# Performance work log

Measured on AMD Instinct MI355X. Metric: run time of the kernel, lower is better.

The kernel has to match this reference:

```python
import jax, jax.numpy as jnp
import numpy as np
from jax import lax

N_CLASS = 21          # VOC: 20 foreground + background
SCORE_THRESH = 0.05   # 'evaluate' preset
NMS_THRESH = 0.3


def loc2bbox(src_bbox, loc):
    # src_bbox, loc: [N, 4] in (y1, x1, y2, x2) / (dy, dx, dh, dw)
    h = src_bbox[:, 2] - src_bbox[:, 0]
    w = src_bbox[:, 3] - src_bbox[:, 1]
    cy = src_bbox[:, 0] + 0.5 * h
    cx = src_bbox[:, 1] + 0.5 * w
    dy, dx, dh, dw = loc[:, 0], loc[:, 1], loc[:, 2], loc[:, 3]
    ncy = dy * h + cy
    ncx = dx * w + cx
    nh = jnp.exp(dh) * h
    nw = jnp.exp(dw) * w
    return jnp.stack([ncy - 0.5 * nh, ncx - 0.5 * nw,
                      ncy + 0.5 * nh, ncx + 0.5 * nw], axis=1)


def pairwise_iou(boxes):
    # boxes: [R, 4] (y1, x1, y2, x2) -> [R, R]
    area = (boxes[:, 2] - boxes[:, 0]) * (boxes[:, 3] - boxes[:, 1])
    ty1 = jnp.maximum(boxes[:, None, 0], boxes[None, :, 0])
    tx1 = jnp.maximum(boxes[:, None, 1], boxes[None, :, 1])
    ty2 = jnp.minimum(boxes[:, None, 2], boxes[None, :, 2])
    tx2 = jnp.minimum(boxes[:, None, 3], boxes[None, :, 3])
    inter = jnp.clip(ty2 - ty1, 0) * jnp.clip(tx2 - tx1, 0)
    union = area[:, None] + area[None, :] - inter
    return inter / jnp.maximum(union, 1e-10)


def nms_keep(boxes, scores):
    # boxes [R,4], scores [R] for one class. Returns bool keep mask [R]
    # (score-thresholded + greedy NMS), fixed shape (mask instead of gather).
    R = boxes.shape[0]
    valid = scores > SCORE_THRESH
    order = jnp.argsort(-scores)
    b = boxes[order]
    v = valid[order]
    suppress = pairwise_iou(b) > NMS_THRESH  # [R, R]
    idx = jnp.arange(R)

    def body(i, keep):
        sup_by_earlier = jnp.any(keep & suppress[:, i] & (idx < i))
        return keep.at[i].set(v[i] & ~sup_by_earlier)

    keep_sorted = lax.fori_loop(0, R, body, jnp.zeros((R,), bool))
    return jnp.zeros((R,), bool).at[order].set(keep_sorted)


def setup_inputs() -> dict:
    key = jax.random.key(0)
    k1, k2, k3, k4 = jax.random.split(key, 4)
    R = 2000
    size_h, size_w = 600, 800
    roi_cls_loc = jax.random.normal(k1, (R, N_CLASS * 4), jnp.float32)
    roi_scores = jax.random.normal(k2, (R, N_CLASS), jnp.float32)
    # valid (y1, x1, y2, x2) rois inside the image
    yx = jax.random.uniform(k3, (R, 2), jnp.float32) * jnp.array([size_h - 32.0, size_w - 32.0])
    hw = 16.0 + jax.random.uniform(k4, (R, 2), jnp.float32) * 128.0
    rois = jnp.concatenate([yx, yx + hw], axis=1)
    return {"roi_cls_loc": roi_cls_loc, "roi_scores": roi_scores,
            "rois": rois, "size_h": size_h, "size_w": size_w}


def reference(roi_cls_loc, roi_scores, rois, size_h, size_w):
    R = rois.shape[0]
    mean = jnp.tile(jnp.asarray([0.0, 0.0, 0.0, 0.0], roi_cls_loc.dtype), N_CLASS)
    std = jnp.tile(jnp.asarray([0.1, 0.1, 0.2, 0.2], roi_cls_loc.dtype), N_CLASS)
    loc = roi_cls_loc * std + mean                      # [R, 4*C]
    loc = loc.reshape(R * N_CLASS, 4)
    src = jnp.broadcast_to(rois[:, None, :], (R, N_CLASS, 4)).reshape(R * N_CLASS, 4)
    box = loc2bbox(src, loc).reshape(R, N_CLASS, 4)
    # clamp y coords (0,2) to [0, H], x coords (1,3) to [0, W]
    y = jnp.clip(box[..., 0::2], 0.0, float(size_h))
    x = jnp.clip(box[..., 1::2], 0.0, float(size_w))
    box = jnp.stack([y[..., 0], x[..., 0], y[..., 1], x[..., 1]], axis=-1)
    prob = jax.nn.softmax(roi_scores, axis=1)           # [R, C]
    # foreground classes only (skip background class 0)
    cls_box = jnp.transpose(box[:, 1:, :], (1, 0, 2))   # [C-1, R, 4]
    cls_prob = prob[:, 1:].T                            # [C-1, R]
    keep = jax.vmap(nms_keep)(lax.stop_gradient(cls_box),
                              lax.stop_gradient(cls_prob))  # [C-1, R] bool
    kept = keep.astype(box.dtype)[..., None]
    # fixed-shape detections: per-class boxes + score, zeroed where suppressed
    out = jnp.concatenate([cls_box * kept, cls_prob[..., None] * kept], axis=-1)
    return out  # [C-1, R, 5]
```

## Files before the change

### kernel.cpp

```cpp
#include <hip/hip_runtime.h>
#include <math.h>

#define NCLS 21
#define NCO 20
#define SUB 8
#define TPB 256
#define RCAP 2048
#define RMAX 2000
#define LDSW 7680
#define SCORE_THRESH 0.05f

typedef unsigned long long u64;
typedef unsigned int u32;
typedef unsigned short u16;

#define IOU_MID (20132661.0 / 67108864.0)

__device__ __forceinline__ u64 readlane64(u64 v, int l) {
    u32 lo = (u32)__builtin_amdgcn_readlane((int)(u32)v, l);
    u32 hi = (u32)__builtin_amdgcn_readlane((int)(u32)(v >> 32), l);
    return ((u64)hi << 32) | lo;
}
__device__ __forceinline__ float readlanef(float v, int l) {
    return __uint_as_float((u32)__builtin_amdgcn_readlane((int)__float_as_uint(v), l));
}
__device__ __forceinline__ u64 shflxor64(u64 v, int m) {
    u32 lo = (u32)__shfl_xor((int)(u32)v, m, 64);
    u32 hi = (u32)__shfl_xor((int)(u32)(v >> 32), m, 64);
    return ((u64)hi << 32) | lo;
}

__device__ __forceinline__ int coff(int ic, int nw) {
    return ((ic * nw - ((ic * (ic - 1)) >> 1)) << 6);
}

__device__ __forceinline__ void decode_box(
    const float* __restrict__ rois, const float* __restrict__ loc,
    int r, int cls, float sh, float sw,
    float& by1, float& bx1, float& by2, float& bx2)
{
    float4 rb = *(const float4*)(rois + r * 4);
    float y1 = rb.x, x1 = rb.y, y2 = rb.z, x2 = rb.w;
    float h = y2 - y1, w = x2 - x1;
    float cy = y1 + 0.5f * h, cx = x1 + 0.5f * w;
    float4 l4 = *(const float4*)(loc + r * (NCLS * 4) + cls * 4);
    float dy = l4.x * 0.1f, dx = l4.y * 0.1f;
    float dh = l4.z * 0.2f, dw = l4.w * 0.2f;
    float ncy = dy * h + cy, ncx = dx * w + cx;
    float nh = expf(dh) * h, nw = expf(dw) * w;
    by1 = fminf(fmaxf(ncy - 0.5f * nh, 0.f), sh);
    bx1 = fminf(fmaxf(ncx - 0.5f * nw, 0.f), sw);
    by2 = fminf(fmaxf(ncy + 0.5f * nh, 0.f), sh);
    bx2 = fminf(fmaxf(ncx + 0.5f * nw, 0.f), sw);
}

__device__ __forceinline__ float softmax_p(
    const float* __restrict__ scores, int r, int cls)
{
    const float* srow = scores + r * NCLS;
    float s[NCLS];
    float4 a0 = *(const float4*)(srow);
    float4 a1 = *(const float4*)(srow + 4);
    float4 a2 = *(const float4*)(srow + 8);
    float4 a3 = *(const float4*)(srow + 12);
    float4 a4 = *(const float4*)(srow + 16);
    s[0]=a0.x; s[1]=a0.y; s[2]=a0.z; s[3]=a0.w;
    s[4]=a1.x; s[5]=a1.y; s[6]=a1.z; s[7]=a1.w;
    s[8]=a2.x; s[9]=a2.y; s[10]=a2.z; s[11]=a2.w;
    s[12]=a3.x; s[13]=a3.y; s[14]=a3.z; s[15]=a3.w;
    s[16]=a4.x; s[17]=a4.y; s[18]=a4.z; s[19]=a4.w;
    s[20]=srow[20];
    float m = -INFINITY;
#pragma unroll
    for (int k = 0; k < NCLS; ++k) m = fmaxf(m, s[k]);
    float sum = 0.f, ec = 0.f;
#pragma unroll
    for (int k = 0; k < NCLS; ++k) {
        float e = expf(s[k] - m);
        sum += e;
        if (k == cls) ec = e;
    }
    return ec / sum;
}

__global__ __launch_bounds__(256) void keygen_kernel(
    const float* __restrict__ scores, u64* __restrict__ ukey,
    int* __restrict__ cntA, int R)
{
    __shared__ u64 lkey[256];
    __shared__ int cnt;
    const int t = threadIdx.x;
    const int c = blockIdx.x >> 3;
    const int s = blockIdx.x & 7;
    const int lane = t & 63;
    if (t == 0) cnt = 0;
    __syncthreads();
    const int rpb = (R + 7) >> 3;
    const int r0 = s * rpb, r1 = min(R, r0 + rpb);
    for (int r = r0 + t; r < r1; r += 256) {
        float p = softmax_p(scores, r, c + 1);
        bool valid = (p > SCORE_THRESH);
        u64 key = ((u64)(~__float_as_uint(p)) << 32) | (u32)r;
        u64 bal = __ballot(valid);
        if (bal) {
            int nb = (int)__popcll(bal);
            int base = 0;
            if (lane == 0) base = atomicAdd(&cnt, nb);
            base = __shfl(base, 0, 64);
            if (valid)
                lkey[base + (int)__popcll(bal & ((1ull << lane) - 1ull))] = key;
        }
    }
    __syncthreads();
    const int n = cnt;
    if (t == 0) cntA[(c << 3) | s] = n;
    for (int j = t; j < n; j += 256)
        ukey[((size_t)c << 11) + (s << 8) + j] = lkey[j];
}

__global__ __launch_bounds__(512) void rank_kernel(
    const float* __restrict__ loc, const float* __restrict__ rois,
    const int* __restrict__ ph, const int* __restrict__ pw,
    const u64* __restrict__ ukey, const int* __restrict__ cntA,
    u64* __restrict__ ord, int* __restrict__ nvv,
    float4* __restrict__ pbG, float* __restrict__ arG, int R)
{
    __shared__ __align__(16) u64 vkey[RCAP + 2];
    const int t = threadIdx.x;
    const int c = blockIdx.x >> 3;
    const int s = blockIdx.x & 7;
    const int wv = t >> 6, lane = t & 63;
    int nv = 0, bseg = 0, nseg = 0;
#pragma unroll
    for (int k = 0; k < 8; ++k) {
        int ck = cntA[(c << 3) | k];
        if (k < wv) bseg += ck;
        if (k == wv) nseg = ck;
        nv += ck;
    }
    for (int j = lane; j < nseg; j += 64)
        vkey[bseg + j] = ukey[((size_t)c << 11) + (wv << 8) + j];
    if (t == 0) vkey[nv] = ~0ull;
    __syncthreads();

    const int sl = (nv + 7) >> 3;
    const int i0 = s * sl;
    const int nmy = max(0, min(nv - i0, sl));
    if (t < nmy) {
        u64 kk = vkey[i0 + t];
        int rank = 0;
        const ulonglong2* vk2 = (const ulonglong2*)vkey;
        const int nj2 = (nv + 1) >> 1;
#pragma unroll 8
        for (int j = 0; j < nj2; ++j) {
            ulonglong2 kj = vk2[j];
            rank += (int)(kj.x < kk) + (int)(kj.y < kk);
        }
        const float sh = (float)(*ph), sw = (float)(*pw);
        int r = (int)(u32)kk;
        float b0, b1, b2, b3;
        decode_box(rois, loc, r, c + 1, sh, sw, b0, b1, b2, b3);
        ord[((size_t)c << 11) + rank] = kk;
        pbG[((size_t)c << 11) + rank] = make_float4(b0, b1, b2, b3);
        arG[((size_t)c << 11) + rank] = (b2 - b0) * (b3 - b1);
    }
    if (t == 0 && s == 0) nvv[c] = nv;
}

__global__ __launch_bounds__(512) void maskp_kernel(
    const float4* __restrict__ pbG, const float* __restrict__ arG,
    const int* __restrict__ nvv, u64* __restrict__ M)
{
    __shared__ float4 pb[RCAP];
    __shared__ float ar[RCAP];
    const int t = threadIdx.x;
    const int c = blockIdx.x >> 3;
    const int s = blockIdx.x & 7;
    const int lane = t & 63;
    const int nv = nvv[c];
    const int nw = (nv + 63) >> 6;
    for (int i = t; i < nv; i += 512) {
        pb[i] = pbG[((size_t)c << 11) + i];
        ar[i] = arG[((size_t)c << 11) + i];
    }
    __syncthreads();

    const int wid = (s << 3) | (t >> 6);
    const int ntasks = nw * (nw + 1) / 2;
    u64* Mc = M + ((size_t)c << 16);
    for (int task = wid; task < ntasks; task += SUB * 8) {
        int ic = 0, rm = task;
        while (rm >= nw - ic) { rm -= nw - ic; ++ic; }
        int v = ic + rm;
        int i = (ic << 6) + lane;
        float4 a = pb[i];
        float iarea = ar[i];
        float4 rj = pb[(v << 6) + lane];
        float ja_l = ar[(v << 6) + lane];
        int jcnt = min(64, nv - (v << 6));
        u64 m = 0;
        for (int jj = 0; jj < jcnt; ++jj) {
            float jy1 = readlanef(rj.x, jj);
            float jx1 = readlanef(rj.y, jj);
            float jy2 = readlanef(rj.z, jj);
            float jx2 = readlanef(rj.w, jj);
            float ja  = readlanef(ja_l, jj);
            float ty1 = fmaxf(a.x, jy1);
            float tx1 = fmaxf(a.y, jx1);
            float ty2 = fminf(a.z, jy2);
            float tx2 = fminf(a.w, jx2);
            float inter = fmaxf(ty2 - ty1, 0.f) * fmaxf(tx2 - tx1, 0.f);
            float uni = fmaxf(iarea + ja - inter, 1e-10f);
            if ((double)inter > IOU_MID * (double)uni) m |= 1ull << jj;
        }
        if (v == ic) m &= (lane < 63) ? (~0ull << (lane + 1)) : 0ull;
        int W = nw - ic;
        if (i < nv) Mc[coff(ic, nw) + lane * W + (v - ic)] = m;
    }
}

__global__ __launch_bounds__(TPB) void resolveout_kernel(
    const float* __restrict__ loc, const float* __restrict__ rois,
    const int* __restrict__ ph, const int* __restrict__ pw,
    const u64* __restrict__ ord, const int* __restrict__ nvv,
    const u64* __restrict__ M, float* __restrict__ out, int R)
{
    __shared__ u64 mlds[LDSW];
    __shared__ u64 keptw[32];
    const int t = threadIdx.x;
    const int c = blockIdx.x >> 3;
    const int s = blockIdx.x & 7;
    const int nv = nvv[c];
    const int nw = (nv + 63) >> 6;
    const u64* Mc = M + ((size_t)c << 16);
    const int S = coff(nw, nw);
    const bool lds_ok = (S <= LDSW);
    if (t < 32) keptw[t] = 0;

    if (lds_ok) {
        for (int base = 0; base < S; base += 2048) {
            u64 v[8];
#pragma unroll
            for (int j = 0; j < 8; ++j) {
                int k = base + (j << 8) + t;
                v[j] = (k < S) ? Mc[k] : 0ull;
            }
#pragma unroll
            for (int j = 0; j < 8; ++j) {
                int k = base + (j << 8) + t;
                if (k < S) mlds[k] = v[j];
            }
        }
    }
    __syncthreads();

    if (t < 64) {
        const int lane = t;
        auto core = [&](const auto* B) {
            u64 remreg = 0;
            for (int w = 0; w < nw; ++w) {
                const int W = nw - w;
                const int cb = coff(w, nw);
                int i = (w << 6) + lane;
                u64 cw = (i < nv) ? B[cb + lane * W] : 0ull;
                int remn = nv - (w << 6);
                u64 vb = (remn >= 64) ? ~0ull : ((1ull << remn) - 1ull);
                u64 cand = vb & ~readlane64(remreg, w);
                u64 X = cand;
                if (X) {
                    for (int it = 0; it < 64; ++it) {
                        u64 contrib = ((X >> lane) & 1ull) ? cw : 0ull;
#pragma unroll
                        for (int d = 1; d < 64; d <<= 1)
                            contrib |= shflxor64(contrib, d);
                        bool keep = ((cand >> lane) & 1ull) &&
                                    !((contrib >> lane) & 1ull);
                        u64 Xn = __ballot(keep);
                        if (Xn == X) break;
                        X = Xn;
                    }
                    if (lane == 0) keptw[w] = X;
                    bool lact = (lane > w) && (lane < nw);
                    u64 km = X, acc = 0;
                    while (km) {
                        int bs[8];
#pragma unroll
                        for (int g = 0; g < 8; ++g) {
                            bs[g] = km ? (__ffsll(km) - 1) : -1;
                            if (km) km &= km - 1;
                        }
                        u64 tmp[8];
#pragma unroll
                        for (int g = 0; g < 8; ++g)
                            tmp[g] = (bs[g] >= 0 && lact)
                                ? B[cb + bs[g] * W + (lane - w)] : 0ull;
#pragma unroll
                        for (int g = 0; g < 8; ++g) acc |= tmp[g];
                    }
                    if (lact) remreg |= acc;
                }
            }
        };
        if (lds_ok) core(mlds); else core(Mc);
    }
    __syncthreads();

    const int chunk = (R + 7) >> 3;
    const int r0 = s * chunk;
    const int r1 = min(R, r0 + chunk);
    float* slice = out + (size_t)c * R * 5;
    for (int k = r0 * 5 + t; k < r1 * 5; k += TPB) slice[k] = 0.f;
    __syncthreads();

    const float sh = (float)(*ph), sw = (float)(*pw);
    for (int i = t; i < nv; i += TPB) {
        if ((keptw[i >> 6] >> (i & 63)) & 1ull) {
            u64 key = ord[((size_t)c << 11) + i];
            int r = (int)(u32)key;
            if (r >= r0 && r < r1) {
                float v0, v1, v2, v3;
                decode_box(rois, loc, r, c + 1, sh, sw, v0, v1, v2, v3);
                float* p = slice + (size_t)r * 5;
                p[0] = v0; p[1] = v1; p[2] = v2; p[3] = v3;
                p[4] = __uint_as_float(~(u32)(key >> 32));
            }
        }
    }
}

#define NTH 1024
__global__ __launch_bounds__(NTH) void fused_kernel(
    const float* __restrict__ loc, const float* __restrict__ scores,
    const float* __restrict__ rois, const int* __restrict__ ph,
    const int* __restrict__ pw, float* __restrict__ out, int R)
{
    __shared__ u64 vkey[RMAX];
    __shared__ float2 p1[RMAX], p2[RMAX];
    __shared__ u64 chunk[64 * 33];
    __shared__ u64 rem[32];
    __shared__ int cnt;

    const int t = threadIdx.x;
    const int lane = t & 63;
    const int c = blockIdx.x + 1;
    const float sh = (float)(*ph), sw = (float)(*pw);

    if (t == 0) cnt = 0;
    if (t < 32) rem[t] = 0;
    __syncthreads();

    for (int r = t; r < R; r += NTH) {
        float p = softmax_p(scores, r, c);
        if (p > SCORE_THRESH) {
            int j = atomicAdd(&cnt, 1);
            vkey[j] = ((u64)(~__float_as_uint(p)) << 32) | (u32)r;
        }
    }
    __syncthreads();
    const int nv = cnt;
    const int nw = (nv + 63) >> 6;

    u64 kk0 = 0, kk1 = 0;
    int r0 = 0, r1 = 0;
    bool in0 = (t < nv), in1 = (t + NTH < nv);
    if (in0) kk0 = vkey[t];
    if (in1) kk1 = vkey[t + NTH];
#pragma unroll 8
    for (int i = 0; i < nv; ++i) {
        u64 k = vkey[i];
        r0 += (k < kk0);
        r1 += (k < kk1);
    }
    __syncthreads();

    for (int u = 0; u < 2; ++u) {
        bool act = u ? in1 : in0;
        if (act) {
            u64 kk = u ? kk1 : kk0;
            int rank = u ? r1 : r0;
            int r = (int)(kk & 0xffffffffu);
            float b0, b1, b2, b3;
            decode_box(rois, loc, r, c, sh, sw, b0, b1, b2, b3);
            vkey[rank] = kk;
            p1[rank] = make_float2(b0, b1);
            p2[rank] = make_float2(b2, b3);
        }
    }
    __syncthreads();

    for (int w = 0; w < nw; ++w) {
        int nwr = nw - w;
        u64 remw = rem[w];
        for (int task = t; task < (nwr << 6); task += NTH) {
            int vr = task >> 6, il = task & 63;
            int i = (w << 6) + il;
            u64 m = 0;
            if (i < nv && !((remw >> il) & 1ull)) {
                int v = w + vr;
                u64 rv = rem[v];
                if (~rv != 0ull) {
                    float2 a1 = p1[i], a2 = p2[i];
                    float iarea = (a2.x - a1.x) * (a2.y - a1.y);
                    int j0 = v << 6;
                    int jhi = min(64, nv - j0);
#pragma unroll 4
                    for (int jj = 0; jj < jhi; ++jj) {
                        float2 b1 = p1[j0 + jj], b2 = p2[j0 + jj];
                        float ty1 = fmaxf(a1.x, b1.x);
                        float tx1 = fmaxf(a1.y, b1.y);
                        float ty2 = fminf(a2.x, b2.x);
                        float tx2 = fminf(a2.y, b2.y);
                        float inter = fmaxf(ty2 - ty1, 0.f) * fmaxf(tx2 - tx1, 0.f);
                        float jarea = (b2.x - b1.x) * (b2.y - b1.y);
                        float uni = fmaxf(iarea + jarea - inter, 1e-10f);
                        if ((double)inter > IOU_MID * (double)uni) m |= 1ull << jj;
                    }
                    if (vr == 0)
                        m &= (il < 63) ? (~0ull << (il + 1)) : 0ull;
                }
            }
            chunk[il * 33 + vr] = m;
        }
        __syncthreads();

        u64 cand = chunk[lane * 33];
        u64 cur = rem[w];
        int remn = nv - (w << 6);
        u64 vb = (remn >= 64) ? ~0ull : ((1ull << remn) - 1ull);
        u64 avail = vb & ~cur;
        u64 kept = 0;
        while (avail) {
            int bb = __ffsll(avail) - 1;
            kept |= 1ull << bb;
            cur |= __shfl(cand, bb, 64);
            avail &= ~(cur | (1ull << bb));
        }
        int vr = t & 31, pg = t >> 5;
        if (vr >= 1 && vr < nwr) {
            u64 acc = 0, km = kept;
            int n = 0;
            while (km) {
                int bb = __ffsll(km) - 1;
                km &= km - 1;
                if ((n & 31) == pg) acc |= chunk[bb * 33 + vr];
                ++n;
            }
            if (acc) atomicOr(&rem[w + vr], acc);
        }
        if (t == 0) rem[w] = cur;
        __syncthreads();
    }

    u16* inv = (u16*)chunk;
    for (int r = t; r < R; r += NTH) inv[r] = 0xffffu;
    __syncthreads();
    for (int i = t; i < nv; i += NTH)
        if (!((rem[i >> 6] >> (i & 63)) & 1ull))
            inv[(int)(vkey[i] & 0xffffffffu)] = (u16)i;
    __syncthreads();
    float* slice = out + (size_t)(c - 1) * R * 5;
    for (int r = t; r < R; r += NTH) {
        int i = inv[r];
        float v0 = 0.f, v1 = 0.f, v2 = 0.f, v3 = 0.f, v4 = 0.f;
        if (i != 0xffff) {
            float2 a1 = p1[i], a2 = p2[i];
            v0 = a1.x; v1 = a1.y; v2 = a2.x; v3 = a2.y;
            v4 = __uint_as_float(~(u32)(vkey[i] >> 32));
        }
        float* p = slice + (size_t)r * 5;
        p[0] = v0; p[1] = v1; p[2] = v2; p[3] = v3; p[4] = v4;
    }
}

extern "C" void kernel_launch(void* const* d_in, const int* in_sizes, int n_in,
                              void* d_out, int out_size, void* d_ws, size_t ws_size,
                              hipStream_t stream) {
    const float* loc    = (const float*)d_in[0];
    const float* scores = (const float*)d_in[1];
    const float* rois   = (const float*)d_in[2];
    const int*   ph     = (const int*)d_in[3];
    const int*   pw     = (const int*)d_in[4];
    float* out = (float*)d_out;
    int R = in_sizes[2] / 4;

    size_t needM    = (size_t)NCO * RCAP * 32 * 8;
    size_t needOrd  = (size_t)NCO * RCAP * 8;
    size_t needUkey = (size_t)NCO * RCAP * 8;
    size_t needPbG  = (size_t)NCO * RCAP * 16;
    size_t needArG  = (size_t)NCO * RCAP * 4;
    size_t need     = needM + needOrd + needUkey + needPbG + needArG + 2048;

    if (R <= RCAP && ws_size >= need) {
        char* w     = (char*)d_ws;
        u64* M      = (u64*)w;                               w += needM;
        u64* ordp   = (u64*)w;                               w += needOrd;
        u64* ukey   = (u64*)w;                               w += needUkey;
        float4* pbG = (float4*)w;                            w += needPbG;
        float* arG  = (float*)w;                             w += needArG;
        int* cntA   = (int*)w;                               w += 1024;
        int* nvv    = (int*)w;
        keygen_kernel<<<NCO * SUB, 256, 0, stream>>>(scores, ukey, cntA, R);
        rank_kernel<<<NCO * SUB, 512, 0, stream>>>(loc, rois, ph, pw, ukey,
                                                   cntA, ordp, nvv, pbG, arG, R);
        maskp_kernel<<<NCO * SUB, 512, 0, stream>>>(pbG, arG, nvv, M);
        resolveout_kernel<<<NCO * SUB, TPB, 0, stream>>>(loc, rois, ph, pw,
                                                         ordp, nvv, M, out, R);
    } else if (R <= RMAX) {
        fused_kernel<<<NCO, NTH, 0, stream>>>(loc, scores, rois, ph, pw, out, R);
    }
}
```

Measured before the change: 116.8 us.

## Fuse four NMS phase kernels into one cooperative kernel with grid syncs

Replaces the sequence of keygen, rank, mask and resolve/output launches with a single cooperative kernel that runs all phases and separates them with grid-wide barriers. The aim is to remove the per-launch overhead and the inter-kernel gaps between the four launches. The cost is grid.sync latency, and every block must now fit the 512-thread shape with about 61 KB of LDS. If the cooperative launch fails, the code falls back to the old four-kernel path.

```diff
diff --git a/kernel.cpp b/kernel.cpp
--- a/kernel.cpp
+++ b/kernel.cpp
@@ -1,5 +1,8 @@
 #include <hip/hip_runtime.h>
+#include <hip/hip_cooperative_groups.h>
 #include <math.h>
+
+namespace cg = cooperative_groups;
 
 #define NCLS 21
 #define NCO 20
@@ -81,6 +84,241 @@
         if (k == cls) ec = e;
     }
     return ec / sum;
+}
+
+__global__ __launch_bounds__(512) void allphase_kernel(
+    const float* __restrict__ loc, const float* __restrict__ scores,
+    const float* __restrict__ rois, const int* __restrict__ ph,
+    const int* __restrict__ pw, u64* __restrict__ ukey,
+    int* __restrict__ cntA, u64* __restrict__ ord,
+    float4* __restrict__ pbG, float* __restrict__ arG,
+    u64* __restrict__ M, float* __restrict__ out, int R)
+{
+    cg::grid_group grid = cg::this_grid();
+    __shared__ __align__(16) char shraw[61440];
+    __shared__ u64 keptw[32];
+    __shared__ int cnt;
+    u64* vkey  = (u64*)shraw;
+    float4* pb = (float4*)shraw;
+    float* ar  = (float*)(shraw + 32768);
+    u64* mlds  = (u64*)shraw;
+
+    const int t = threadIdx.x;
+    const int c = blockIdx.x >> 3;
+    const int s = blockIdx.x & 7;
+    const int lane = t & 63;
+    const int wv = t >> 6;
+
+    if (t == 0) cnt = 0;
+    __syncthreads();
+    {
+        const int rpb = (R + 7) >> 3;
+        const int r0k = s * rpb, r1k = min(R, r0k + rpb);
+        u64* useg = ukey + ((size_t)c << 11) + (s << 8);
+        for (int r = r0k + t; r < r1k; r += 512) {
+            float p = softmax_p(scores, r, c + 1);
+            bool valid = (p > SCORE_THRESH);
+            u64 key = ((u64)(~__float_as_uint(p)) << 32) | (u32)r;
+            u64 bal = __ballot(valid);
+            if (bal) {
+                int nb = (int)__popcll(bal);
+                int base = 0;
+                if (lane == 0) base = atomicAdd(&cnt, nb);
+                base = __shfl(base, 0, 64);
+                if (valid)
+                    useg[base + (int)__popcll(bal & ((1ull << lane) - 1ull))] = key;
+            }
+        }
+        __syncthreads();
+        if (t == 0) cntA[(c << 3) | s] = cnt;
+    }
+    grid.sync();
+
+    int nv = 0;
+    {
+        int bseg = 0, nseg = 0;
+#pragma unroll
+        for (int k = 0; k < 8; ++k) {
+            int ck = cntA[(c << 3) | k];
+            if (k < wv) bseg += ck;
+            if (k == wv) nseg = ck;
+            nv += ck;
+        }
+        for (int j = lane; j < nseg; j += 64)
+            vkey[bseg + j] = ukey[((size_t)c << 11) + (wv << 8) + j];
+        if (t == 0) vkey[nv] = ~0ull;
+        __syncthreads();
+
+        const int sl = (nv + 7) >> 3;
+        const int i0 = s * sl;
+        const int nmy = max(0, min(nv - i0, sl));
+        const int q = t & 3;
+        const ulonglong2* vk2 = (const ulonglong2*)vkey;
+        const int nj2 = (nv + 1) >> 1;
+        const int jb0 = (q * nj2) >> 2;
+        const int jb1 = ((q + 1) * nj2) >> 2;
+        const float shf = (float)(*ph), swf = (float)(*pw);
+        for (int il = (t >> 2); il < nmy; il += 128) {
+            u64 kk = vkey[i0 + il];
+            int rank = 0;
+#pragma unroll 8
+            for (int j = jb0; j < jb1; ++j) {
+                ulonglong2 kj = vk2[j];
+                rank += (int)(kj.x < kk) + (int)(kj.y < kk);
+            }
+            rank += __shfl_xor(rank, 1, 64);
+            rank += __shfl_xor(rank, 2, 64);
+            if (q == 0) {
+                int r = (int)(u32)kk;
+                float b0, b1, b2, b3;
+                decode_box(rois, loc, r, c + 1, shf, swf, b0, b1, b2, b3);
+                ord[((size_t)c << 11) + rank] = kk;
+                pbG[((size_t)c << 11) + rank] = make_float4(b0, b1, b2, b3);
+                arG[((size_t)c << 11) + rank] = (b2 - b0) * (b3 - b1);
+            }
+        }
+    }
+    grid.sync();
+
+    const int nw = (nv + 63) >> 6;
+    {
+        for (int i = t; i < nv; i += 512) {
+            pb[i] = pbG[((size_t)c << 11) + i];
+            ar[i] = arG[((size_t)c << 11) + i];
+        }
+        __syncthreads();
+
+        const int wid = (s << 3) | (t >> 6);
+        const int ntasks = nw * (nw + 1) / 2;
+        u64* Mc = M + ((size_t)c << 16);
+        for (int task = wid; task < ntasks; task += SUB * 8) {
+            int ic = 0, rm = task;
+            while (rm >= nw - ic) { rm -= nw - ic; ++ic; }
+            int v = ic + rm;
+            int i = (ic << 6) + lane;
+            float4 a = pb[i];
+            float iarea = ar[i];
+            float4 rj = pb[(v << 6) + lane];
+            float ja_l = ar[(v << 6) + lane];
+            int jcnt = min(64, nv - (v << 6));
+            u64 m = 0;
+            for (int jj = 0; jj < jcnt; ++jj) {
+                float jy1 = readlanef(rj.x, jj);
+                float jx1 = readlanef(rj.y, jj);
+                float jy2 = readlanef(rj.z, jj);
+                float jx2 = readlanef(rj.w, jj);
+                float ja  = readlanef(ja_l, jj);
+                float ty1 = fmaxf(a.x, jy1);
+                float tx1 = fmaxf(a.y, jx1);
+                float ty2 = fminf(a.z, jy2);
+                float tx2 = fminf(a.w, jx2);
+                float inter = fmaxf(ty2 - ty1, 0.f) * fmaxf(tx2 - tx1, 0.f);
+                float uni = fmaxf(iarea + ja - inter, 1e-10f);
+                if ((double)inter > IOU_MID * (double)uni) m |= 1ull << jj;
+            }
+            if (v == ic) m &= (lane < 63) ? (~0ull << (lane + 1)) : 0ull;
+            int W = nw - ic;
+            if (i < nv) Mc[coff(ic, nw) + lane * W + (v - ic)] = m;
+        }
+    }
+    grid.sync();
+
+    {
+        const u64* Mc = M + ((size_t)c << 16);
+        const int S = coff(nw, nw);
+        const bool lds_ok = (S <= LDSW);
+        if (t < 32) keptw[t] = 0;
+
+        if (lds_ok) {
+            for (int base = 0; base < S; base += 4096) {
+                u64 v[8];
+#pragma unroll
+                for (int j = 0; j < 8; ++j) {
+                    int k = base + (j << 9) + t;
+                    v[j] = (k < S) ? Mc[k] : 0ull;
+                }
+#pragma unroll
+                for (int j = 0; j < 8; ++j) {
+                    int k = base + (j << 9) + t;
+                    if (k < S) mlds[k] = v[j];
+                }
+            }
+        }
+        __syncthreads();
+
+        if (t < 64) {
+            const int lane64 = t;
+            auto core = [&](const auto* B) {
+                u64 remreg = 0;
+                for (int w = 0; w < nw; ++w) {
+                    const int W = nw - w;
+                    const int cb = coff(w, nw);
+                    int i = (w << 6) + lane64;
+                    u64 cw = (i < nv) ? B[cb + lane64 * W] : 0ull;
+                    int remn = nv - (w << 6);
+                    u64 vb = (remn >= 64) ? ~0ull : ((1ull << remn) - 1ull);
+                    u64 cand = vb & ~readlane64(remreg, w);
+                    u64 X = cand;
+                    if (X) {
+                        for (int it = 0; it < 64; ++it) {
+                            u64 contrib = ((X >> lane64) & 1ull) ? cw : 0ull;
+#pragma unroll
+                            for (int d = 1; d < 64; d <<= 1)
+                                contrib |= shflxor64(contrib, d);
+                            bool keep = ((cand >> lane64) & 1ull) &&
+                                        !((contrib >> lane64) & 1ull);
+                            u64 Xn = __ballot(keep);
+                            if (Xn == X) break;
+                            X = Xn;
+                        }
+                        if (lane64 == 0) keptw[w] = X;
+                        bool lact = (lane64 > w) && (lane64 < nw);
+                        u64 km = X, acc = 0;
+                        while (km) {
+                            int bs[8];
+#pragma unroll
+                            for (int g = 0; g < 8; ++g) {
+                                bs[g] = km ? (__ffsll(km) - 1) : -1;
+                                if (km) km &= km - 1;
+                            }
+                            u64 tmp[8];
+#pragma unroll
+                            for (int g = 0; g < 8; ++g)
+                                tmp[g] = (bs[g] >= 0 && lact)
+                                    ? B[cb + bs[g] * W + (lane64 - w)] : 0ull;
+#pragma unroll
+                            for (int g = 0; g < 8; ++g) acc |= tmp[g];
+                        }
+                        if (lact) remreg |= acc;
+                    }
+                }
+            };
+            if (lds_ok) core(mlds); else core(Mc);
+        }
+        __syncthreads();
+
+        const int chunkR = (R + 7) >> 3;
+        const int rr0 = s * chunkR;
+        const int rr1 = min(R, rr0 + chunkR);
+        float* slice = out + (size_t)c * R * 5;
+        for (int k = rr0 * 5 + t; k < rr1 * 5; k += 512) slice[k] = 0.f;
+        __syncthreads();
+
+        const float sh2 = (float)(*ph), sw2 = (float)(*pw);
+        for (int i = t; i < nv; i += 512) {
+            if ((keptw[i >> 6] >> (i & 63)) & 1ull) {
+                u64 key = ord[((size_t)c << 11) + i];
+                int r = (int)(u32)key;
+                if (r >= rr0 && r < rr1) {
+                    float v0, v1, v2, v3;
+                    decode_box(rois, loc, r, c + 1, sh2, sw2, v0, v1, v2, v3);
+                    float* p = slice + (size_t)r * 5;
+                    p[0] = v0; p[1] = v1; p[2] = v2; p[3] = v3;
+                    p[4] = __uint_as_float(~(u32)(key >> 32));
+                }
+            }
+        }
+    }
 }
 
 __global__ __launch_bounds__(256) void keygen_kernel(
@@ -499,12 +737,26 @@
         float* arG  = (float*)w;                             w += needArG;
         int* cntA   = (int*)w;                               w += 1024;
         int* nvv    = (int*)w;
-        keygen_kernel<<<NCO * SUB, 256, 0, stream>>>(scores, ukey, cntA, R);
-        rank_kernel<<<NCO * SUB, 512, 0, stream>>>(loc, rois, ph, pw, ukey,
-                                                   cntA, ordp, nvv, pbG, arG, R);
-        maskp_kernel<<<NCO * SUB, 512, 0, stream>>>(pbG, arG, nvv, M);
-        resolveout_kernel<<<NCO * SUB, TPB, 0, stream>>>(loc, rois, ph, pw,
-                                                         ordp, nvv, M, out, R);
+
+        void* args[] = {
+            (void*)&loc, (void*)&scores, (void*)&rois, (void*)&ph, (void*)&pw,
+            (void*)&ukey, (void*)&cntA, (void*)&ordp, (void*)&pbG, (void*)&arG,
+            (void*)&M, (void*)&out, (void*)&R
+        };
+        hipError_t e = hipLaunchCooperativeKernel(
+            (const void*)allphase_kernel, dim3(NCO * SUB), dim3(512),
+            args, 0, stream);
+        if (e != hipSuccess) {
+            (void)hipGetLastError();
+            keygen_kernel<<<NCO * SUB, 256, 0, stream>>>(scores, ukey, cntA, R);
+            rank_kernel<<<NCO * SUB, 512, 0, stream>>>(loc, rois, ph, pw, ukey,
+                                                       cntA, ordp, nvv, pbG,
+                                                       arG, R);
+            maskp_kernel<<<NCO * SUB, 512, 0, stream>>>(pbG, arG, nvv, M);
+            resolveout_kernel<<<NCO * SUB, TPB, 0, stream>>>(loc, rois, ph, pw,
+                                                             ordp, nvv, M, out,
+                                                             R);
+        }
     } else if (R <= RMAX) {
         fused_kernel<<<NCO, NTH, 0, stream>>>(loc, scores, rois, ph, pw, out, R);
     }
```

Result: slower. 180.0 us (+54.2%).

## Fuse four NMS kernels into one persistent kernel with per-class spin barriers

Applied to the files above, without the earlier changes.

Replaces the keygen, rank, mask and resolve launches with a single 160-block kernel. The eight blocks of each class meet at flag barriers in global memory, using atomics and spinning, so three kernel boundaries and their launch gaps disappear. The rank step is also split across four threads per key, with a shuffle reduction to combine the partial counts. In exchange it adds a memset launch, relies on all 160 blocks being resident at once to avoid deadlock, and shares one aliased LDS buffer between phases.

```diff
diff --git a/kernel.cpp b/kernel.cpp
--- a/kernel.cpp
+++ b/kernel.cpp
@@ -4,11 +4,11 @@
 #define NCLS 21
 #define NCO 20
 #define SUB 8
-#define TPB 256
 #define RCAP 2048
 #define RMAX 2000
 #define LDSW 7680
 #define SCORE_THRESH 0.05f
+#define MAGIC 0x5A17C0DE
 
 typedef unsigned long long u64;
 typedef unsigned int u32;
@@ -83,246 +83,252 @@
     return ec / sum;
 }
 
-__global__ __launch_bounds__(256) void keygen_kernel(
-    const float* __restrict__ scores, u64* __restrict__ ukey,
-    int* __restrict__ cntA, int R)
+__global__ __launch_bounds__(512) void allsync_kernel(
+    const float* __restrict__ loc, const float* __restrict__ scores,
+    const float* __restrict__ rois, const int* __restrict__ ph,
+    const int* __restrict__ pw, u64* __restrict__ ukey,
+    int* __restrict__ cntA, u64* __restrict__ ord,
+    float4* __restrict__ pbG, float* __restrict__ arG,
+    u64* __restrict__ M, int* __restrict__ flg,
+    float* __restrict__ out, int R)
 {
-    __shared__ u64 lkey[256];
+    __shared__ __align__(16) char shraw[61440];
+    __shared__ u64 keptw[32];
     __shared__ int cnt;
+    u64* vkey  = (u64*)shraw;
+    float4* pb = (float4*)shraw;
+    float* ar  = (float*)(shraw + 32768);
+    u64* mlds  = (u64*)shraw;
+
     const int t = threadIdx.x;
     const int c = blockIdx.x >> 3;
     const int s = blockIdx.x & 7;
     const int lane = t & 63;
+    const int wv = t >> 6;
+
+    auto classync = [&](int* f) {
+        __syncthreads();
+        if (t == 0) {
+            __threadfence();
+            __hip_atomic_store(&f[(c << 3) | s], MAGIC, __ATOMIC_RELEASE,
+                               __HIP_MEMORY_SCOPE_AGENT);
+        }
+        if (t < 8) {
+            while (__hip_atomic_load(&f[(c << 3) | t], __ATOMIC_RELAXED,
+                                     __HIP_MEMORY_SCOPE_AGENT) != MAGIC)
+                __builtin_amdgcn_s_sleep(1);
+        }
+        __syncthreads();
+        __threadfence();
+    };
+
     if (t == 0) cnt = 0;
     __syncthreads();
-    const int rpb = (R + 7) >> 3;
-    const int r0 = s * rpb, r1 = min(R, r0 + rpb);
-    for (int r = r0 + t; r < r1; r += 256) {
-        float p = softmax_p(scores, r, c + 1);
-        bool valid = (p > SCORE_THRESH);
-        u64 key = ((u64)(~__float_as_uint(p)) << 32) | (u32)r;
-        u64 bal = __ballot(valid);
-        if (bal) {
-            int nb = (int)__popcll(bal);
-            int base = 0;
-            if (lane == 0) base = atomicAdd(&cnt, nb);
-            base = __shfl(base, 0, 64);
-            if (valid)
-                lkey[base + (int)__popcll(bal & ((1ull << lane) - 1ull))] = key;
-        }
-    }
-    __syncthreads();
-    const int n = cnt;
-    if (t == 0) cntA[(c << 3) | s] = n;
-    for (int j = t; j < n; j += 256)
-        ukey[((size_t)c << 11) + (s << 8) + j] = lkey[j];
-}
-
-__global__ __launch_bounds__(512) void rank_kernel(
-    const float* __restrict__ loc, const float* __restrict__ rois,
-    const int* __restrict__ ph, const int* __restrict__ pw,
-    const u64* __restrict__ ukey, const int* __restrict__ cntA,
-    u64* __restrict__ ord, int* __restrict__ nvv,
-    float4* __restrict__ pbG, float* __restrict__ arG, int R)
-{
-    __shared__ __align__(16) u64 vkey[RCAP + 2];
-    const int t = threadIdx.x;
-    const int c = blockIdx.x >> 3;
-    const int s = blockIdx.x & 7;
-    const int wv = t >> 6, lane = t & 63;
-    int nv = 0, bseg = 0, nseg = 0;
-#pragma unroll
-    for (int k = 0; k < 8; ++k) {
-        int ck = cntA[(c << 3) | k];
-        if (k < wv) bseg += ck;
-        if (k == wv) nseg = ck;
-        nv += ck;
-    }
-    for (int j = lane; j < nseg; j += 64)
-        vkey[bseg + j] = ukey[((size_t)c << 11) + (wv << 8) + j];
-    if (t == 0) vkey[nv] = ~0ull;
-    __syncthreads();
-
-    const int sl = (nv + 7) >> 3;
-    const int i0 = s * sl;
-    const int nmy = max(0, min(nv - i0, sl));
-    if (t < nmy) {
-        u64 kk = vkey[i0 + t];
-        int rank = 0;
+    {
+        const int rpb = (R + 7) >> 3;
+        const int r0k = s * rpb, r1k = min(R, r0k + rpb);
+        u64* useg = ukey + ((size_t)c << 11) + (s << 8);
+        for (int r = r0k + t; r < r1k; r += 512) {
+            float p = softmax_p(scores, r, c + 1);
+            bool valid = (p > SCORE_THRESH);
+            u64 key = ((u64)(~__float_as_uint(p)) << 32) | (u32)r;
+            u64 bal = __ballot(valid);
+            if (bal) {
+                int nb = (int)__popcll(bal);
+                int base = 0;
+                if (lane == 0) base = atomicAdd(&cnt, nb);
+                base = __shfl(base, 0, 64);
+                if (valid)
+                    useg[base + (int)__popcll(bal & ((1ull << lane) - 1ull))] = key;
+            }
+        }
+        __syncthreads();
+        if (t == 0) cntA[(c << 3) | s] = cnt;
+    }
+    classync(flg);
+
+    int nv = 0;
+    {
+        int bseg = 0, nseg = 0;
+#pragma unroll
+        for (int k = 0; k < 8; ++k) {
+            int ck = cntA[(c << 3) | k];
+            if (k < wv) bseg += ck;
+            if (k == wv) nseg = ck;
+            nv += ck;
+        }
+        for (int j = lane; j < nseg; j += 64)
+            vkey[bseg + j] = ukey[((size_t)c << 11) + (wv << 8) + j];
+        if (t == 0) vkey[nv] = ~0ull;
+        __syncthreads();
+
+        const int sl = (nv + 7) >> 3;
+        const int i0 = s * sl;
+        const int nmy = max(0, min(nv - i0, sl));
+        const int q = t & 3;
         const ulonglong2* vk2 = (const ulonglong2*)vkey;
         const int nj2 = (nv + 1) >> 1;
+        const int jb0 = (q * nj2) >> 2;
+        const int jb1 = ((q + 1) * nj2) >> 2;
+        const float shf = (float)(*ph), swf = (float)(*pw);
+        for (int il = (t >> 2); il < nmy; il += 128) {
+            u64 kk = vkey[i0 + il];
+            int rank = 0;
 #pragma unroll 8
-        for (int j = 0; j < nj2; ++j) {
-            ulonglong2 kj = vk2[j];
-            rank += (int)(kj.x < kk) + (int)(kj.y < kk);
-        }
-        const float sh = (float)(*ph), sw = (float)(*pw);
-        int r = (int)(u32)kk;
-        float b0, b1, b2, b3;
-        decode_box(rois, loc, r, c + 1, sh, sw, b0, b1, b2, b3);
-        ord[((size_t)c << 11) + rank] = kk;
-        pbG[((size_t)c << 11) + rank] = make_float4(b0, b1, b2, b3);
-        arG[((size_t)c << 11) + rank] = (b2 - b0) * (b3 - b1);
-    }
-    if (t == 0 && s == 0) nvv[c] = nv;
-}
-
-__global__ __launch_bounds__(512) void maskp_kernel(
-    const float4* __restrict__ pbG, const float* __restrict__ arG,
-    const int* __restrict__ nvv, u64* __restrict__ M)
-{
-    __shared__ float4 pb[RCAP];
-    __shared__ float ar[RCAP];
-    const int t = threadIdx.x;
-    const int c = blockIdx.x >> 3;
-    const int s = blockIdx.x & 7;
-    const int lane = t & 63;
-    const int nv = nvv[c];
+            for (int j = jb0; j < jb1; ++j) {
+                ulonglong2 kj = vk2[j];
+                rank += (int)(kj.x < kk) + (int)(kj.y < kk);
+            }
+            rank += __shfl_xor(rank, 1, 64);
+            rank += __shfl_xor(rank, 2, 64);
+            if (q == 0) {
+                int r = (int)(u32)kk;
+                float b0, b1, b2, b3;
+                decode_box(rois, loc, r, c + 1, shf, swf, b0, b1, b2, b3);
+                ord[((size_t)c << 11) + rank] = kk;
+                pbG[((size_t)c << 11) + rank] = make_float4(b0, b1, b2, b3);
+                arG[((size_t)c << 11) + rank] = (b2 - b0) * (b3 - b1);
+            }
+        }
+    }
+    classync(flg + 256);
+
     const int nw = (nv + 63) >> 6;
-    for (int i = t; i < nv; i += 512) {
-        pb[i] = pbG[((size_t)c << 11) + i];
-        ar[i] = arG[((size_t)c << 11) + i];
-    }
-    __syncthreads();
-
-    const int wid = (s << 3) | (t >> 6);
-    const int ntasks = nw * (nw + 1) / 2;
-    u64* Mc = M + ((size_t)c << 16);
-    for (int task = wid; task < ntasks; task += SUB * 8) {
-        int ic = 0, rm = task;
-        while (rm >= nw - ic) { rm -= nw - ic; ++ic; }
-        int v = ic + rm;
-        int i = (ic << 6) + lane;
-        float4 a = pb[i];
-        float iarea = ar[i];
-        float4 rj = pb[(v << 6) + lane];
-        float ja_l = ar[(v << 6) + lane];
-        int jcnt = min(64, nv - (v << 6));
-        u64 m = 0;
-        for (int jj = 0; jj < jcnt; ++jj) {
-            float jy1 = readlanef(rj.x, jj);
-            float jx1 = readlanef(rj.y, jj);
-            float jy2 = readlanef(rj.z, jj);
-            float jx2 = readlanef(rj.w, jj);
-            float ja  = readlanef(ja_l, jj);
-            float ty1 = fmaxf(a.x, jy1);
-            float tx1 = fmaxf(a.y, jx1);
-            float ty2 = fminf(a.z, jy2);
-            float tx2 = fminf(a.w, jx2);
-            float inter = fmaxf(ty2 - ty1, 0.f) * fmaxf(tx2 - tx1, 0.f);
-            float uni = fmaxf(iarea + ja - inter, 1e-10f);
-            if ((double)inter > IOU_MID * (double)uni) m |= 1ull << jj;
-        }
-        if (v == ic) m &= (lane < 63) ? (~0ull << (lane + 1)) : 0ull;
-        int W = nw - ic;
-        if (i < nv) Mc[coff(ic, nw) + lane * W + (v - ic)] = m;
-    }
-}
-
-__global__ __launch_bounds__(TPB) void resolveout_kernel(
-    const float* __restrict__ loc, const float* __restrict__ rois,
-    const int* __restrict__ ph, const int* __restrict__ pw,
-    const u64* __restrict__ ord, const int* __restrict__ nvv,
-    const u64* __restrict__ M, float* __restrict__ out, int R)
-{
-    __shared__ u64 mlds[LDSW];
-    __shared__ u64 keptw[32];
-    const int t = threadIdx.x;
-    const int c = blockIdx.x >> 3;
-    const int s = blockIdx.x & 7;
-    const int nv = nvv[c];
-    const int nw = (nv + 63) >> 6;
-    const u64* Mc = M + ((size_t)c << 16);
-    const int S = coff(nw, nw);
-    const bool lds_ok = (S <= LDSW);
-    if (t < 32) keptw[t] = 0;
-
-    if (lds_ok) {
-        for (int base = 0; base < S; base += 2048) {
-            u64 v[8];
-#pragma unroll
-            for (int j = 0; j < 8; ++j) {
-                int k = base + (j << 8) + t;
-                v[j] = (k < S) ? Mc[k] : 0ull;
-            }
-#pragma unroll
-            for (int j = 0; j < 8; ++j) {
-                int k = base + (j << 8) + t;
-                if (k < S) mlds[k] = v[j];
-            }
-        }
-    }
-    __syncthreads();
-
-    if (t < 64) {
-        const int lane = t;
-        auto core = [&](const auto* B) {
-            u64 remreg = 0;
-            for (int w = 0; w < nw; ++w) {
-                const int W = nw - w;
-                const int cb = coff(w, nw);
-                int i = (w << 6) + lane;
-                u64 cw = (i < nv) ? B[cb + lane * W] : 0ull;
-                int remn = nv - (w << 6);
-                u64 vb = (remn >= 64) ? ~0ull : ((1ull << remn) - 1ull);
-                u64 cand = vb & ~readlane64(remreg, w);
-                u64 X = cand;
-                if (X) {
-                    for (int it = 0; it < 64; ++it) {
-                        u64 contrib = ((X >> lane) & 1ull) ? cw : 0ull;
-#pragma unroll
-                        for (int d = 1; d < 64; d <<= 1)
-                            contrib |= shflxor64(contrib, d);
-                        bool keep = ((cand >> lane) & 1ull) &&
-                                    !((contrib >> lane) & 1ull);
-                        u64 Xn = __ballot(keep);
-                        if (Xn == X) break;
-                        X = Xn;
+    {
+        for (int i = t; i < nv; i += 512) {
+            pb[i] = pbG[((size_t)c << 11) + i];
+            ar[i] = arG[((size_t)c << 11) + i];
+        }
+        __syncthreads();
+
+        const int wid = (s << 3) | (t >> 6);
+        const int ntasks = nw * (nw + 1) / 2;
+        u64* Mc = M + ((size_t)c << 16);
+        for (int task = wid; task < ntasks; task += SUB * 8) {
+            int ic = 0, rm = task;
+            while (rm >= nw - ic) { rm -= nw - ic; ++ic; }
+            int v = ic + rm;
+            int i = (ic << 6) + lane;
+            float4 a = pb[i];
+            float iarea = ar[i];
+            float4 rj = pb[(v << 6) + lane];
+            float ja_l = ar[(v << 6) + lane];
+            int jcnt = min(64, nv - (v << 6));
+            u64 m = 0;
+            for (int jj = 0; jj < jcnt; ++jj) {
+                float jy1 = readlanef(rj.x, jj);
+                float jx1 = readlanef(rj.y, jj);
+                float jy2 = readlanef(rj.z, jj);
+                float jx2 = readlanef(rj.w, jj);
+                float ja  = readlanef(ja_l, jj);
+                float ty1 = fmaxf(a.x, jy1);
+                float tx1 = fmaxf(a.y, jx1);
+                float ty2 = fminf(a.z, jy2);
+                float tx2 = fminf(a.w, jx2);
+                float inter = fmaxf(ty2 - ty1, 0.f) * fmaxf(tx2 - tx1, 0.f);
+                float uni = fmaxf(iarea + ja - inter, 1e-10f);
+                if ((double)inter > IOU_MID * (double)uni) m |= 1ull << jj;
+            }
+            if (v == ic) m &= (lane < 63) ? (~0ull << (lane + 1)) : 0ull;
+            int W = nw - ic;
+            if (i < nv) Mc[coff(ic, nw) + lane * W + (v - ic)] = m;
+        }
+    }
+    classync(flg + 512);
+
+    {
+        const u64* Mc = M + ((size_t)c << 16);
+        const int S = coff(nw, nw);
+        const bool lds_ok = (S <= LDSW);
+        if (t < 32) keptw[t] = 0;
+
+        if (lds_ok) {
+            for (int base = 0; base < S; base += 4096) {
+                u64 v[8];
+#pragma unroll
+                for (int j = 0; j < 8; ++j) {
+                    int k = base + (j << 9) + t;
+                    v[j] = (k < S) ? Mc[k] : 0ull;
+                }
+#pragma unroll
+                for (int j = 0; j < 8; ++j) {
+                    int k = base + (j << 9) + t;
+                    if (k < S) mlds[k] = v[j];
+                }
+            }
+        }
+        __syncthreads();
+
+        if (t < 64) {
+            const int lane64 = t;
+            auto core = [&](const auto* B) {
+                u64 remreg = 0;
+                for (int w = 0; w < nw; ++w) {
+                    const int W = nw - w;
+                    const int cb = coff(w, nw);
+                    int i = (w << 6) + lane64;
+                    u64 cw = (i < nv) ? B[cb + lane64 * W] : 0ull;
+                    int remn = nv - (w << 6);
+                    u64 vb = (remn >= 64) ? ~0ull : ((1ull << remn) - 1ull);
+                    u64 cand = vb & ~readlane64(remreg, w);
+                    u64 X = cand;
+                    if (X) {
+                        for (int it = 0; it < 64; ++it) {
+                            u64 contrib = ((X >> lane64) & 1ull) ? cw : 0ull;
+#pragma unroll
+                            for (int d = 1; d < 64; d <<= 1)
+                                contrib |= shflxor64(contrib, d);
+                            bool keep = ((cand >> lane64) & 1ull) &&
+                                        !((contrib >> lane64) & 1ull);
+                            u64 Xn = __ballot(keep);
+                            if (Xn == X) break;
+                            X = Xn;
+                        }
+                        if (lane64 == 0) keptw[w] = X;
+                        bool lact = (lane64 > w) && (lane64 < nw);
+                        u64 km = X, acc = 0;
+                        while (km) {
+                            int bs[8];
+#pragma unroll
+                            for (int g = 0; g < 8; ++g) {
+                                bs[g] = km ? (__ffsll(km) - 1) : -1;
+                                if (km) km &= km - 1;
+                            }
+                            u64 tmp[8];
+#pragma unroll
+                            for (int g = 0; g < 8; ++g)
+                                tmp[g] = (bs[g] >= 0 && lact)
+                                    ? B[cb + bs[g] * W + (lane64 - w)] : 0ull;
+#pragma unroll
+                            for (int g = 0; g < 8; ++g) acc |= tmp[g];
+                        }
+                        if (lact) remreg |= acc;
                     }
-                    if (lane == 0) keptw[w] = X;
-                    bool lact = (lane > w) && (lane < nw);
-                    u64 km = X, acc = 0;
-                    while (km) {
-                        int bs[8];
-#pragma unroll
-                        for (int g = 0; g < 8; ++g) {
-                            bs[g] = km ? (__ffsll(km) - 1) : -1;
-                            if (km) km &= km - 1;
-                        }
-                        u64 tmp[8];
-#pragma unroll
-                        for (int g = 0; g < 8; ++g)
-                            tmp[g] = (bs[g] >= 0 && lact)
-                                ? B[cb + bs[g] * W + (lane - w)] : 0ull;
-#pragma unroll
-                        for (int g = 0; g < 8; ++g) acc |= tmp[g];
-                    }
-                    if (lact) remreg |= acc;
                 }
-            }
-        };
-        if (lds_ok) core(mlds); else core(Mc);
-    }
-    __syncthreads();
-
-    const int chunk = (R + 7) >> 3;
-    const int r0 = s * chunk;
-    const int r1 = min(R, r0 + chunk);
-    float* slice = out + (size_t)c * R * 5;
-    for (int k = r0 * 5 + t; k < r1 * 5; k += TPB) slice[k] = 0.f;
-    __syncthreads();
-
-    const float sh = (float)(*ph), sw = (float)(*pw);
-    for (int i = t; i < nv; i += TPB) {
-        if ((keptw[i >> 6] >> (i & 63)) & 1ull) {
-            u64 key = ord[((size_t)c << 11) + i];
-            int r = (int)(u32)key;
-            if (r >= r0 && r < r1) {
-                float v0, v1, v2, v3;
-                decode_box(rois, loc, r, c + 1, sh, sw, v0, v1, v2, v3);
-                float* p = slice + (size_t)r * 5;
-                p[0] = v0; p[1] = v1; p[2] = v2; p[3] = v3;
-                p[4] = __uint_as_float(~(u32)(key >> 32));
+            };
+            if (lds_ok) core(mlds); else core(Mc);
+        }
+        __syncthreads();
+
+        const int chunkR = (R + 7) >> 3;
+        const int rr0 = s * chunkR;
+        const int rr1 = min(R, rr0 + chunkR);
+        float* slice = out + (size_t)c * R * 5;
+        for (int k = rr0 * 5 + t; k < rr1 * 5; k += 512) slice[k] = 0.f;
+        __syncthreads();
+
+        const float sh2 = (float)(*ph), sw2 = (float)(*pw);
+        for (int i = t; i < nv; i += 512) {
+            if ((keptw[i >> 6] >> (i & 63)) & 1ull) {
+                u64 key = ord[((size_t)c << 11) + i];
+                int r = (int)(u32)key;
+                if (r >= rr0 && r < rr1) {
+                    float v0, v1, v2, v3;
+                    decode_box(rois, loc, r, c + 1, sh2, sw2, v0, v1, v2, v3);
+                    float* p = slice + (size_t)r * 5;
+                    p[0] = v0; p[1] = v1; p[2] = v2; p[3] = v3;
+                    p[4] = __uint_as_float(~(u32)(key >> 32));
+                }
             }
         }
     }
@@ -488,7 +494,7 @@
     size_t needUkey = (size_t)NCO * RCAP * 8;
     size_t needPbG  = (size_t)NCO * RCAP * 16;
     size_t needArG  = (size_t)NCO * RCAP * 4;
-    size_t need     = needM + needOrd + needUkey + needPbG + needArG + 2048;
+    size_t need     = needM + needOrd + needUkey + needPbG + needArG + 8192;
 
     if (R <= RCAP && ws_size >= need) {
         char* w     = (char*)d_ws;
@@ -498,13 +504,12 @@
         float4* pbG = (float4*)w;                            w += needPbG;
         float* arG  = (float*)w;                             w += needArG;
         int* cntA   = (int*)w;                               w += 1024;
-        int* nvv    = (int*)w;
-        keygen_kernel<<<NCO * SUB, 256, 0, stream>>>(scores, ukey, cntA, R);
-        rank_kernel<<<NCO * SUB, 512, 0, stream>>>(loc, rois, ph, pw, ukey,
-                                                   cntA, ordp, nvv, pbG, arG, R);
-        maskp_kernel<<<NCO * SUB, 512, 0, stream>>>(pbG, arG, nvv, M);
-        resolveout_kernel<<<NCO * SUB, TPB, 0, stream>>>(loc, rois, ph, pw,
-                                                         ordp, nvv, M, out, R);
+        int* flg    = (int*)w;
+
+        hipMemsetAsync(flg, 0, 3 * 256 * sizeof(int), stream);
+        allsync_kernel<<<NCO * SUB, 512, 0, stream>>>(
+            loc, scores, rois, ph, pw, ukey, cntA, ordp, pbG, arG, M, flg,
+            out, R);
     } else if (R <= RMAX) {
         fused_kernel<<<NCO, NTH, 0, stream>>>(loc, scores, rois, ph, pw, out, R);
     }
```

Result: slower. 180.7 us (+54.7%).

## Fuse rank sort and IoU mask kernels with redundant per-block ranking

Applied to the files above, without the earlier changes.

Merges the rank kernel and the mask-building kernel into one launch. Each of the 8 blocks per class now computes the full sorted order itself, using four threads per key that split the comparison range and combine counts with shuffles, and it decodes every box straight into shared memory. This removes one kernel launch and the global round trip for the sorted boxes and areas. In exchange every block repeats the full ranking and box decode work for its class, roughly 8 times the original rank work.

```diff
diff --git a/kernel.cpp b/kernel.cpp
--- a/kernel.cpp
+++ b/kernel.cpp
@@ -83,7 +83,7 @@
     return ec / sum;
 }
 
-__global__ __launch_bounds__(256) void keygen_kernel(
+__global__ __launch_bounds__(TPB) void keygen_kernel(
     const float* __restrict__ scores, u64* __restrict__ ukey,
     int* __restrict__ cntA, int R)
 {
@@ -118,70 +118,64 @@
         ukey[((size_t)c << 11) + (s << 8) + j] = lkey[j];
 }
 
-__global__ __launch_bounds__(512) void rank_kernel(
+__global__ __launch_bounds__(512) void sortmaskp_kernel(
     const float* __restrict__ loc, const float* __restrict__ rois,
     const int* __restrict__ ph, const int* __restrict__ pw,
     const u64* __restrict__ ukey, const int* __restrict__ cntA,
     u64* __restrict__ ord, int* __restrict__ nvv,
-    float4* __restrict__ pbG, float* __restrict__ arG, int R)
+    u64* __restrict__ M, int R)
 {
     __shared__ __align__(16) u64 vkey[RCAP + 2];
-    const int t = threadIdx.x;
-    const int c = blockIdx.x >> 3;
-    const int s = blockIdx.x & 7;
-    const int wv = t >> 6, lane = t & 63;
-    int nv = 0, bseg = 0, nseg = 0;
-#pragma unroll
-    for (int k = 0; k < 8; ++k) {
-        int ck = cntA[(c << 3) | k];
-        if (k < wv) bseg += ck;
-        if (k == wv) nseg = ck;
-        nv += ck;
-    }
-    for (int j = lane; j < nseg; j += 64)
-        vkey[bseg + j] = ukey[((size_t)c << 11) + (wv << 8) + j];
-    if (t == 0) vkey[nv] = ~0ull;
-    __syncthreads();
-
-    const int sl = (nv + 7) >> 3;
-    const int i0 = s * sl;
-    const int nmy = max(0, min(nv - i0, sl));
-    if (t < nmy) {
-        u64 kk = vkey[i0 + t];
-        int rank = 0;
-        const ulonglong2* vk2 = (const ulonglong2*)vkey;
-        const int nj2 = (nv + 1) >> 1;
-#pragma unroll 8
-        for (int j = 0; j < nj2; ++j) {
-            ulonglong2 kj = vk2[j];
-            rank += (int)(kj.x < kk) + (int)(kj.y < kk);
-        }
-        const float sh = (float)(*ph), sw = (float)(*pw);
-        int r = (int)(u32)kk;
-        float b0, b1, b2, b3;
-        decode_box(rois, loc, r, c + 1, sh, sw, b0, b1, b2, b3);
-        ord[((size_t)c << 11) + rank] = kk;
-        pbG[((size_t)c << 11) + rank] = make_float4(b0, b1, b2, b3);
-        arG[((size_t)c << 11) + rank] = (b2 - b0) * (b3 - b1);
-    }
-    if (t == 0 && s == 0) nvv[c] = nv;
-}
-
-__global__ __launch_bounds__(512) void maskp_kernel(
-    const float4* __restrict__ pbG, const float* __restrict__ arG,
-    const int* __restrict__ nvv, u64* __restrict__ M)
-{
     __shared__ float4 pb[RCAP];
     __shared__ float ar[RCAP];
     const int t = threadIdx.x;
     const int c = blockIdx.x >> 3;
     const int s = blockIdx.x & 7;
     const int lane = t & 63;
-    const int nv = nvv[c];
+    const int wv = t >> 6;
+
+    int nv = 0, bseg = 0, nseg = 0;
+#pragma unroll
+    for (int k = 0; k < 8; ++k) {
+        int ck = cntA[(c << 3) | k];
+        if (k < wv) bseg += ck;
+        if (k == wv) nseg = ck;
+        nv += ck;
+    }
+    for (int j = lane; j < nseg; j += 64)
+        vkey[bseg + j] = ukey[((size_t)c << 11) + (wv << 8) + j];
+    if (t == 0) vkey[nv] = ~0ull;
+    __syncthreads();
+
     const int nw = (nv + 63) >> 6;
-    for (int i = t; i < nv; i += 512) {
-        pb[i] = pbG[((size_t)c << 11) + i];
-        ar[i] = arG[((size_t)c << 11) + i];
+
+    {
+        const int q = t & 3;
+        const ulonglong2* vk2 = (const ulonglong2*)vkey;
+        const int nj2 = (nv + 1) >> 1;
+        const int jb0 = (q * nj2) >> 2;
+        const int jb1 = ((q + 1) * nj2) >> 2;
+        const float shf = (float)(*ph), swf = (float)(*pw);
+        for (int il = (t >> 2); il < nv; il += 128) {
+            u64 kk = vkey[il];
+            int rank = 0;
+#pragma unroll 8
+            for (int j = jb0; j < jb1; ++j) {
+                ulonglong2 kj = vk2[j];
+                rank += (int)(kj.x < kk) + (int)(kj.y < kk);
+            }
+            rank += __shfl_xor(rank, 1, 64);
+            rank += __shfl_xor(rank, 2, 64);
+            if (q == 0) {
+                int r = (int)(u32)kk;
+                float b0, b1, b2, b3;
+                decode_box(rois, loc, r, c + 1, shf, swf, b0, b1, b2, b3);
+                pb[rank] = make_float4(b0, b1, b2, b3);
+                ar[rank] = (b2 - b0) * (b3 - b1);
+                if (s == 0) ord[((size_t)c << 11) + rank] = kk;
+            }
+        }
+        if (s == 0 && t == 0) nvv[c] = nv;
     }
     __syncthreads();
 
@@ -486,23 +480,20 @@
     size_t needM    = (size_t)NCO * RCAP * 32 * 8;
     size_t needOrd  = (size_t)NCO * RCAP * 8;
     size_t needUkey = (size_t)NCO * RCAP * 8;
-    size_t needPbG  = (size_t)NCO * RCAP * 16;
-    size_t needArG  = (size_t)NCO * RCAP * 4;
-    size_t need     = needM + needOrd + needUkey + needPbG + needArG + 2048;
+    size_t need     = needM + needOrd + needUkey + 2048;
 
     if (R <= RCAP && ws_size >= need) {
         char* w     = (char*)d_ws;
         u64* M      = (u64*)w;                               w += needM;
         u64* ordp   = (u64*)w;                               w += needOrd;
         u64* ukey   = (u64*)w;                               w += needUkey;
-        float4* pbG = (float4*)w;                            w += needPbG;
-        float* arG  = (float*)w;                             w += needArG;
         int* cntA   = (int*)w;                               w += 1024;
         int* nvv    = (int*)w;
-        keygen_kernel<<<NCO * SUB, 256, 0, stream>>>(scores, ukey, cntA, R);
-        rank_kernel<<<NCO * SUB, 512, 0, stream>>>(loc, rois, ph, pw, ukey,
-                                                   cntA, ordp, nvv, pbG, arG, R);
-        maskp_kernel<<<NCO * SUB, 512, 0, stream>>>(pbG, arG, nvv, M);
+
+        keygen_kernel<<<NCO * SUB, TPB, 0, stream>>>(scores, ukey, cntA, R);
+        sortmaskp_kernel<<<NCO * SUB, 512, 0, stream>>>(loc, rois, ph, pw,
+                                                        ukey, cntA, ordp, nvv,
+                                                        M, R);
         resolveout_kernel<<<NCO * SUB, TPB, 0, stream>>>(loc, rois, ph, pw,
                                                          ordp, nvv, M, out, R);
     } else if (R <= RMAX) {
```

Result: slower. 130.0 us (+11.3%).
